# Kernel tuning notes

Hardware: AMD Instinct MI355X
Metric: run time of the kernel (lower is better)

## Reference

```python
import jax, jax.numpy as jnp
import numpy as np

C = 768      # channel
H = 6        # height = 4 + 2*pre_step
W = 6        # width  = 4 + 2*pre_step
NB = 3       # n_block = H/2
SPLIT = 6    # = width
LS = 1536    # lstm_size = C * H / NB
NH = 4       # attention heads
DM = 512     # attention d_model
DK = DM // NH
B = 256


def setup_inputs() -> dict:
    key = jax.random.key(0)
    ks = jax.random.split(key, 20)
    s_l = 1.0 / np.sqrt(LS)
    s_a = 1.0 / np.sqrt(C)
    s_o = 1.0 / np.sqrt(DM)
    u = lambda k, shape, s: jax.random.uniform(k, shape, jnp.float32, -s, s)
    return {
        "x": jax.random.normal(ks[0], (B, H * W, C), jnp.float32),
        # 2-layer LSTM encoder (input=hidden=LS), torch gate order i,f,g,o
        "enc_Wih": u(ks[1], (2, 4 * LS, LS), s_l),
        "enc_Whh": u(ks[2], (2, 4 * LS, LS), s_l),
        "enc_bih": u(ks[3], (2, 4 * LS), s_l),
        "enc_bhh": u(ks[4], (2, 4 * LS), s_l),
        # 2-layer LSTM decoder
        "dec_Wih": u(ks[5], (2, 4 * LS, LS), s_l),
        "dec_Whh": u(ks[6], (2, 4 * LS, LS), s_l),
        "dec_bih": u(ks[7], (2, 4 * LS), s_l),
        "dec_bhh": u(ks[8], (2, 4 * LS), s_l),
        # multi-head attention: 768 -> 512 (4 heads x 128) -> 768
        "Wq": u(ks[9], (C, DM), s_a), "bq": u(ks[10], (DM,), s_a),
        "Wk": u(ks[11], (C, DM), s_a), "bk": u(ks[12], (DM,), s_a),
        "Wv": u(ks[13], (C, DM), s_a), "bv": u(ks[14], (DM,), s_a),
        "Wo": u(ks[15], (DM, C), s_o), "bo": u(ks[16], (C,), s_o),
        # LayerNorm over channel
        "ln_g": jnp.ones((C,), jnp.float32),
        "ln_b": jnp.zeros((C,), jnp.float32),
    }


def _cell(x, h, c, Wi, Wh, bi, bh):
    g = x @ Wi.T + bi + h @ Wh.T + bh
    i, f, gg, o = jnp.split(g, 4, axis=-1)
    c = jax.nn.sigmoid(f) * c + jax.nn.sigmoid(i) * jnp.tanh(gg)
    h = jax.nn.sigmoid(o) * jnp.tanh(c)
    return h, c


def _step2(st, xt, Wih, Whh, bih, bhh):
    # one timestep of a 2-layer LSTM
    h0, c0, h1, c1 = st
    h0, c0 = _cell(xt, h0, c0, Wih[0], Whh[0], bih[0], bhh[0])
    h1, c1 = _cell(h0, h1, c1, Wih[1], Whh[1], bih[1], bhh[1])
    return (h0, c0, h1, c1), h1


def _forward(x, enc_Wih, enc_Whh, enc_bih, enc_bhh,
             dec_Wih, dec_Whh, dec_bih, dec_bhh,
             Wq, bq, Wk, bk, Wv, bv, Wo, bo, ln_g, ln_b):
    Bx = x.shape[0]
    xb = x.reshape(Bx, NB, 2, W, C)
    # per block, each column j is a single-timestep feature concatenating the 2 rows
    # -> time-major sequence (SPLIT, NB*Bx, LS), blocks folded into the batch dim
    seq = jnp.transpose(xb, (3, 1, 0, 2, 4)).reshape(W, NB * Bx, LS)
    z = jnp.zeros((NB * Bx, LS), x.dtype)
    carry0 = (z, z, z, z)
    # encoder consumes columns in reversed order (j = split-1 .. 0)
    enc_st, enc_ys = jax.lax.scan(
        lambda s, xt: _step2(s, xt, enc_Wih, enc_Whh, enc_bih, enc_bhh),
        carry0, seq[::-1])
    en_out = enc_ys[-1]

    def dec_step(carry, _):
        st, inp = carry
        st, out = _step2(st, inp, dec_Wih, dec_Whh, dec_bih, dec_bhh)
        return (st, out), out
    _, dec_ys = jax.lax.scan(dec_step, (enc_st, en_out), None, length=SPLIT)

    # dec_ys: (SPLIT, NB*Bx, LS) -> xout_total: (NB, Bx, 2, SPLIT, C)
    xout = dec_ys.reshape(SPLIT, NB, Bx, 2, C).transpose(1, 2, 3, 0, 4)
    xt = xout.reshape(NB, Bx, 2 * SPLIT, C)

    # neighbor-block q/k, own-block v (NB=3): i=0 -> (q1,k2,v0); i=1 -> (q0,k2,v1); i=2 -> (q1,k0,v2)
    q = xt[jnp.array([1, 0, 1])]
    k = xt[jnp.array([2, 2, 0])]
    v = xt
    T = 2 * SPLIT
    Q = (q @ Wq + bq).reshape(NB, Bx, T, NH, DK)
    K = (k @ Wk + bk).reshape(NB, Bx, T, NH, DK)
    V = (v @ Wv + bv).reshape(NB, Bx, T, NH, DK)
    scores = jnp.einsum('nbqhd,nbkhd->nbhqk', Q, K) / np.float32(np.sqrt(DK))
    att = jax.nn.softmax(scores, axis=-1)
    o = jnp.einsum('nbhqk,nbkhd->nbqhd', att, V).reshape(NB, Bx, T, DM)
    o = o @ Wo + bo  # (NB, Bx, T, C)

    # concat blocks along height, layernorm over channel
    feat = o.reshape(NB, Bx, 2, W, C).transpose(1, 0, 2, 3, 4).reshape(Bx, H * W, C)
    mu = feat.mean(-1, keepdims=True)
    var = feat.var(-1, keepdims=True)
    feature = (feat - mu) / jnp.sqrt(var + 1e-5) * ln_g + ln_b
    out_decode = feature.reshape(Bx, H, W, C)[:, 1:5, 1:5, :]
    return feature, out_decode


def reference(x, enc_Wih, enc_Whh, enc_bih, enc_bhh,
              dec_Wih, dec_Whh, dec_bih, dec_bhh,
              Wq, bq, Wk, bk, Wv, bv, Wo, bo, ln_g, ln_b):
    return _forward(x, enc_Wih, enc_Whh, enc_bih, enc_bhh,
                    dec_Wih, dec_Whh, dec_bih, dec_bhh,
                    Wq, bq, Wk, bk, Wv, bv, Wo, bo, ln_g, ln_b)
```

## Files before the change

kernel.cpp:

```cpp
#include <hip/hip_runtime.h>


typedef unsigned short u16;
typedef unsigned int   u32;
typedef __bf16 bf16x8 __attribute__((ext_vector_type(8)));
typedef short  short8 __attribute__((ext_vector_type(8)));
typedef float  f32x4  __attribute__((ext_vector_type(4)));

__device__ __forceinline__ u16 f2bf(float f) {
  u32 u = __float_as_uint(f);
  u32 r = u + 0x7FFFu + ((u >> 16) & 1u);
  return (u16)(r >> 16);
}

__device__ __forceinline__ f32x4 mfma16(short8 a, short8 b, f32x4 c) {
  return __builtin_amdgcn_mfma_f32_16x16x32_bf16(
      __builtin_bit_cast(bf16x8, a), __builtin_bit_cast(bf16x8, b), c, 0, 0, 0);
}

__device__ __forceinline__ void gload16(const u16* g, u16* l) {
  __builtin_amdgcn_global_load_lds(
      (const __attribute__((address_space(1))) u32*)g,
      (__attribute__((address_space(3))) u32*)l, 16, 0, 0);
}

__global__ __launch_bounds__(384) void lstm_cell(
    const u16* __restrict__ X, const u16* __restrict__ H,
    const u16* __restrict__ Wih, const u16* __restrict__ Whh,
    const float* __restrict__ bi, const float* __restrict__ bh,
    float* __restrict__ c, u16* __restrict__ hout, u16* __restrict__ h2)
{
  __shared__ __align__(16) u16 smem[36864];
  const int tid  = threadIdx.x;
  const int wid   = (blockIdx.x & 7) * 32 + (blockIdx.x >> 3);
  const int strip = wid >> 3;
  const int bm    = wid & 7;
  const int strip48 = strip * 48;
  const int lane = tid & 63, wave = tid >> 6;
  const int t  = wave % 3;
  const int mh = wave / 3;
  const int r16  = lane & 15, kg = lane >> 4;
  const int srow = lane >> 2, sslot = lane & 3;

  f32x4 acc[3][4];
#pragma unroll
  for (int mi = 0; mi < 3; ++mi)
#pragma unroll
    for (int g = 0; g < 4; ++g) acc[mi][g] = (f32x4)0.0f;

  auto stage = [&](int s) {
    const int slot = s & 3;
    const u16* A = (s < 48) ? X : H;
    const u16* W = (s < 48) ? Wih : Whh;
    const int k0 = ((s < 48) ? s : (s - 48)) << 5;
#pragma unroll
    for (int cc = 0; cc < 3; ++cc) {
      const int call = wave * 3 + cc;
      if (call < 6) {
        const int row  = call * 16 + srow;
        const int slog = sslot ^ ((row >> 1) & 3);
        gload16(A + (size_t)(bm * 96 + row) * 1536 + k0 + slog * 8,
                smem + slot * 3072 + call * 512);
      } else {
        const int rb   = (call - 6) * 16 + srow;
        const int slog = sslot ^ ((rb >> 1) & 3);
        const int g    = (call - 6) / 3;
        const int hh   = rb - g * 48;
        gload16(W + ((size_t)g * 1536 + strip48 + hh) * 1536 + k0 + slog * 8,
                smem + 12288 + slot * 6144 + (call - 6) * 512);
      }
    }
  };

  auto computeFrom = [&](int s) {
    const int slot = s & 3;
    const u16* baseA = smem + slot * 3072;
    const u16* baseB = smem + 12288 + slot * 6144;
    short8 af[3];
#pragma unroll
    for (int mi = 0; mi < 3; ++mi) {
      const int row = mh * 48 + mi * 16 + r16;
      af[mi] = *(const short8*)(baseA + row * 32 + ((kg ^ ((row >> 1) & 3)) << 3));
    }
    short8 bfr[4];
#pragma unroll
    for (int g = 0; g < 4; ++g) {
      const int rb = g * 48 + t * 16 + r16;
      bfr[g] = *(const short8*)(baseB + rb * 32 + ((kg ^ ((rb >> 1) & 3)) << 3));
    }
#pragma unroll
    for (int mi = 0; mi < 3; ++mi)
#pragma unroll
      for (int g = 0; g < 4; ++g)
        acc[mi][g] = mfma16(af[mi], bfr[g], acc[mi][g]);
  };

  stage(0); stage(1); stage(2); stage(3);

  for (int i = 0; i < 92; ++i) {
    asm volatile("s_waitcnt vmcnt(9)" ::: "memory");
    __builtin_amdgcn_sched_barrier(0);
    __builtin_amdgcn_s_barrier();
    computeFrom(i);
    __builtin_amdgcn_s_barrier();
    __builtin_amdgcn_sched_barrier(0);
    stage(i + 4);
  }
  asm volatile("s_waitcnt vmcnt(9)" ::: "memory");
  __builtin_amdgcn_sched_barrier(0);
  __builtin_amdgcn_s_barrier();
  computeFrom(92);
  __builtin_amdgcn_s_barrier();
  asm volatile("s_waitcnt vmcnt(6)" ::: "memory");
  __builtin_amdgcn_sched_barrier(0);
  __builtin_amdgcn_s_barrier();
  computeFrom(93);
  __builtin_amdgcn_s_barrier();
  asm volatile("s_waitcnt vmcnt(3)" ::: "memory");
  __builtin_amdgcn_sched_barrier(0);
  __builtin_amdgcn_s_barrier();
  computeFrom(94);
  __builtin_amdgcn_s_barrier();
  asm volatile("s_waitcnt vmcnt(0)" ::: "memory");
  __builtin_amdgcn_sched_barrier(0);
  __builtin_amdgcn_s_barrier();
  computeFrom(95);

  const int h = strip48 + t * 16 + r16;
  float bsum[4];
#pragma unroll
  for (int g = 0; g < 4; ++g)
    bsum[g] = bi[g * 1536 + h] + bh[g * 1536 + h];
#pragma unroll
  for (int mi = 0; mi < 3; ++mi) {
    const int row0 = bm * 96 + mh * 48 + mi * 16 + kg * 4;
#pragma unroll
    for (int j = 0; j < 4; ++j) {
      const float ig = acc[mi][0][j] + bsum[0];
      const float fg = acc[mi][1][j] + bsum[1];
      const float gz = acc[mi][2][j] + bsum[2];
      const float og = acc[mi][3][j] + bsum[3];
      const float si = 1.0f / (1.0f + expf(-ig));
      const float sf = 1.0f / (1.0f + expf(-fg));
      const float so = 1.0f / (1.0f + expf(-og));
      const size_t cij = (size_t)(row0 + j) * 1536 + h;
      const float cnew = sf * c[cij] + si * tanhf(gz);
      c[cij] = cnew;
      const u16 hv = f2bf(so * tanhf(cnew));
      hout[cij] = hv;
      if (h2) h2[cij] = hv;
    }
  }
}

template <int OUT_BF16, int HAS_BIAS>
__global__ __launch_bounds__(256, 2) void gemm_bt(
    const u16* __restrict__ A1, const u16* __restrict__ B1, int K1,
    const float* __restrict__ bias, void* __restrict__ Cout, int N)
{
  __shared__ __align__(16) u16 smem[16384];
  const int tid  = threadIdx.x;
  const int bn   = blockIdx.x * 128;
  const int bm   = blockIdx.y * 128;
  const int lane = tid & 63, wave = tid >> 6;
  const int wm   = (wave >> 1) * 64, wn = (wave & 1) * 64;
  const int r16  = lane & 15, kg = lane >> 4;
  const int srow = lane >> 2, sslot = lane & 3;

  f32x4 acc[4][4];
#pragma unroll
  for (int i = 0; i < 4; ++i)
#pragma unroll
    for (int j = 0; j < 4; ++j) acc[i][j] = (f32x4)0.0f;

  const int nt = K1 >> 5;
  auto stage = [&](int i, int buf) {
    const int k0 = i << 5;
#pragma unroll
    for (int cc2 = 0; cc2 < 2; ++cc2) {
      const int call = wave * 2 + cc2;
      const int row  = call * 16 + srow;
      const int slog = sslot ^ ((row >> 1) & 3);
      gload16(A1 + (size_t)(bm + row) * K1 + k0 + slog * 8, smem + buf * 4096 + call * 512);
      gload16(B1 + (size_t)(bn + row) * K1 + k0 + slog * 8, smem + 8192 + buf * 4096 + call * 512);
    }
  };

  stage(0, 0);
  __syncthreads();
  int cur = 0;
  for (int i = 0; i < nt; ++i) {
    if (i + 1 < nt) stage(i + 1, cur ^ 1);
    const u16* baseA = smem + cur * 4096;
    const u16* baseB = smem + 8192 + cur * 4096;
    short8 af[4], bfr[4];
#pragma unroll
    for (int mi = 0; mi < 4; ++mi) {
      const int row = wm + mi * 16 + r16;
      af[mi] = *(const short8*)(baseA + row * 32 + ((kg ^ ((row >> 1) & 3)) << 3));
    }
#pragma unroll
    for (int ni = 0; ni < 4; ++ni) {
      const int row = wn + ni * 16 + r16;
      bfr[ni] = *(const short8*)(baseB + row * 32 + ((kg ^ ((row >> 1) & 3)) << 3));
    }
#pragma unroll
    for (int mi = 0; mi < 4; ++mi)
#pragma unroll
      for (int ni = 0; ni < 4; ++ni)
        acc[mi][ni] = mfma16(af[mi], bfr[ni], acc[mi][ni]);
    __syncthreads();
    cur ^= 1;
  }

  const size_t Ns = (size_t)N;
#pragma unroll
  for (int ni = 0; ni < 4; ++ni) {
    const int col = bn + wn + ni * 16 + r16;
    const float bvv = HAS_BIAS ? bias[col] : 0.0f;
#pragma unroll
    for (int mi = 0; mi < 4; ++mi) {
      const int row0 = bm + wm + mi * 16 + kg * 4;
      f32x4 v = acc[mi][ni];
#pragma unroll
      for (int j = 0; j < 4; ++j) {
        const float val = v[j] + bvv;
        const size_t idx = (size_t)(row0 + j) * Ns + col;
        if (OUT_BF16) ((u16*)Cout)[idx] = f2bf(val);
        else          ((float*)Cout)[idx] = val;
      }
    }
  }
}

__global__ __launch_bounds__(256) void attn_kernel(const u16* __restrict__ P, u16* __restrict__ O)
{
  __shared__ __align__(16) u16 sQ[12 * 520];
  __shared__ __align__(16) u16 sK[12 * 520];
  __shared__ __align__(16) u16 sVT[512 * 24];
  __shared__ __align__(16) u16 sS[4 * 16 * 16];
  const int tid = threadIdx.x;
  const int nb = blockIdx.x >> 8;
  const int b  = blockIdx.x & 255;
  const int qb = (nb == 1) ? 0 : 1;
  const int kb = (nb == 2) ? 0 : 2;
  const size_t rq = ((size_t)qb * 256 + b) * 12;
  const size_t rk = ((size_t)kb * 256 + b) * 12;
  const size_t rv = ((size_t)nb * 256 + b) * 12;

  for (int e4 = tid; e4 < 1536; e4 += 256) {
    const int t  = e4 >> 7;
    const int cc = (e4 & 127) * 4;
    uint2 qv = *(const uint2*)(P + (rq + t) * 1536 + cc);
    *(uint2*)(sQ + t * 520 + cc) = qv;
    uint2 kv = *(const uint2*)(P + (rk + t) * 1536 + 512 + cc);
    *(uint2*)(sK + t * 520 + cc) = kv;
    uint2 vv = *(const uint2*)(P + (rv + t) * 1536 + 1024 + cc);
    sVT[(cc + 0) * 24 + t] = (u16)(vv.x & 0xffff);
    sVT[(cc + 1) * 24 + t] = (u16)(vv.x >> 16);
    sVT[(cc + 2) * 24 + t] = (u16)(vv.y & 0xffff);
    sVT[(cc + 3) * 24 + t] = (u16)(vv.y >> 16);
  }
  for (int i = tid; i < 2048; i += 256) sVT[(i >> 2) * 24 + 12 + (i & 3)] = 0;
  __syncthreads();

  const int lane = tid & 63, h = tid >> 6;
  const int r16 = lane & 15, kg = lane >> 4;
  const int hcol = h * 128;

  f32x4 sc = (f32x4)0.0f;
#pragma unroll
  for (int ks = 0; ks < 4; ++ks) {
    short8 aq  = (r16 < 12) ? *(const short8*)(sQ + r16 * 520 + hcol + ks * 32 + kg * 8) : (short8)0;
    short8 bk2 = (r16 < 12) ? *(const short8*)(sK + r16 * 520 + hcol + ks * 32 + kg * 8) : (short8)0;
    sc = mfma16(aq, bk2, sc);
  }
  const float scale = 0.08838834764831845f;
#pragma unroll
  for (int j = 0; j < 4; ++j) {
    float v = (r16 < 12) ? sc[j] * scale : -1e30f;
    float m = v;
#pragma unroll
    for (int d = 1; d < 16; d <<= 1) m = fmaxf(m, __shfl_xor(m, d));
    float e = expf(v - m);
    float s = e;
#pragma unroll
    for (int d = 1; d < 16; d <<= 1) s += __shfl_xor(s, d);
    sS[h * 256 + (kg * 4 + j) * 16 + r16] = f2bf(e / s);
  }
  __syncthreads();
  short8 av = (kg < 2) ? *(const short8*)(sS + h * 256 + r16 * 16 + kg * 8) : (short8)0;
#pragma unroll
  for (int dt = 0; dt < 8; ++dt) {
    short8 bv2 = (kg < 2) ? *(const short8*)(sVT + (hcol + dt * 16 + r16) * 24 + kg * 8) : (short8)0;
    f32x4 ov = mfma16(av, bv2, (f32x4)0.0f);
    if (kg < 3) {
#pragma unroll
      for (int j = 0; j < 4; ++j) {
        const int q = kg * 4 + j;
        O[(rv + q) * 512 + hcol + dt * 16 + r16] = f2bf(ov[j]);
      }
    }
  }
}

__global__ __launch_bounds__(256) void layernorm_kernel(
    const float* __restrict__ feat, const float* __restrict__ gam,
    const float* __restrict__ bet, float* __restrict__ out)
{
  const int row = blockIdx.x;
  const int b = row / 36, hidx = row - b * 36;
  const int nb = hidx / 12, t = hidx - nb * 12;
  const float* src = feat + ((size_t)nb * 3072 + b * 12 + t) * 768;
  const int tid = threadIdx.x;
  float v0 = src[tid], v1 = src[tid + 256], v2 = src[tid + 512];
  float s = v0 + v1 + v2, sq = v0 * v0 + v1 * v1 + v2 * v2;
#pragma unroll
  for (int d = 1; d < 64; d <<= 1) { s += __shfl_xor(s, d); sq += __shfl_xor(sq, d); }
  __shared__ float ps[4], pq[4];
  if ((tid & 63) == 0) { ps[tid >> 6] = s; pq[tid >> 6] = sq; }
  __syncthreads();
  s  = ps[0] + ps[1] + ps[2] + ps[3];
  sq = pq[0] + pq[1] + pq[2] + pq[3];
  const float mean = s * (1.0f / 768.0f);
  const float var  = sq * (1.0f / 768.0f) - mean * mean;
  const float rstd = rsqrtf(var + 1e-5f);
  float* dst = out + (size_t)row * 768;
  const int hh = hidx / 6, wp = hidx - hh * 6;
  float* dst2 = nullptr;
  if (hh >= 1 && hh < 5 && wp >= 1 && wp < 5)
    dst2 = out + 7077888 + ((size_t)b * 16 + (hh - 1) * 4 + (wp - 1)) * 768;
#pragma unroll
  for (int i = 0; i < 3; ++i) {
    const int cix = tid + i * 256;
    const float vv = (i == 0) ? v0 : (i == 1 ? v1 : v2);
    const float o = (vv - mean) * rstd * gam[cix] + bet[cix];
    dst[cix] = o;
    if (dst2) dst2[cix] = o;
  }
}

__global__ __launch_bounds__(256) void cast_bf16_kernel(const float* __restrict__ src,
                                                        u16* __restrict__ dst, int n4)
{
  const int i = blockIdx.x * 256 + threadIdx.x;
  if (i >= n4) return;
  float4 v = ((const float4*)src)[i];
  uint2 pk;
  pk.x = (u32)f2bf(v.x) | ((u32)f2bf(v.y) << 16);
  pk.y = (u32)f2bf(v.z) | ((u32)f2bf(v.w) << 16);
  ((uint2*)dst)[i] = pk;
}

__global__ __launch_bounds__(256) void pack_qkvT(const float* __restrict__ Wq,
    const float* __restrict__ Wk, const float* __restrict__ Wv, u16* __restrict__ dst)
{
  const int idx = blockIdx.x * 256 + threadIdx.x;
  if (idx >= 1536 * 768) return;
  const int d = idx / 768, c = idx - d * 768;
  float v;
  if (d < 512)       v = Wq[(size_t)c * 512 + d];
  else if (d < 1024) v = Wk[(size_t)c * 512 + d - 512];
  else               v = Wv[(size_t)c * 512 + d - 1024];
  dst[idx] = f2bf(v);
}

__global__ __launch_bounds__(256) void pack_bias(const float* __restrict__ bq,
    const float* __restrict__ bk, const float* __restrict__ bv, float* __restrict__ dst)
{
  const int i = blockIdx.x * 256 + threadIdx.x;
  if (i < 512)       dst[i] = bq[i];
  else if (i < 1024) dst[i] = bk[i - 512];
  else if (i < 1536) dst[i] = bv[i - 1024];
}

__global__ __launch_bounds__(256) void pack_WoT(const float* __restrict__ Wo, u16* __restrict__ dst)
{
  const int idx = blockIdx.x * 256 + threadIdx.x;
  if (idx >= 768 * 512) return;
  const int n = idx / 512, k = idx - n * 512;
  dst[idx] = f2bf(Wo[(size_t)k * 768 + n]);
}

__global__ __launch_bounds__(256) void build_Xe(const float* __restrict__ x, u16* __restrict__ Xe)
{
  const int i4 = blockIdx.x * 256 + threadIdx.x;
  if (i4 >= 1769472) return;
  const int e = i4 * 4;
  const int c = e % 768;
  const int r2 = (e / 768) & 1;
  const int r = (e / 1536) % 768;
  const int s = e / 1179648;
  const int nb = r >> 8, bb = r & 255;
  const int w = 5 - s;
  const float* src = x + ((size_t)bb * 36 + (nb * 2 + r2) * 6 + w) * 768 + c;
  float4 v = *(const float4*)src;
  uint2 pk;
  pk.x = (u32)f2bf(v.x) | ((u32)f2bf(v.y) << 16);
  pk.y = (u32)f2bf(v.z) | ((u32)f2bf(v.w) << 16);
  ((uint2*)Xe)[i4] = pk;
}

__global__ __launch_bounds__(256) void build_xt(const u16* __restrict__ decys, u16* __restrict__ xt)
{
  const int i4 = blockIdx.x * 256 + threadIdx.x;
  if (i4 >= 1769472) return;
  const int e = i4 * 4;
  const int c = e % 768;
  const int t = (e / 768) % 12;
  const int b = (e / 9216) % 256;
  const int nb = e / 2359296;
  const int r2 = t / 6, s = t - r2 * 6;
  const u16* src = decys + ((size_t)s * 768 + nb * 256 + b) * 1536 + r2 * 768 + c;
  ((uint2*)xt)[i4] = *(const uint2*)src;
}

extern "C" void kernel_launch(void* const* d_in, const int* in_sizes, int n_in,
                              void* d_out, int out_size, void* d_ws, size_t ws_size,
                              hipStream_t stream)
{
  const float* x    = (const float*)d_in[0];
  const float* eWih = (const float*)d_in[1];
  const float* eWhh = (const float*)d_in[2];
  const float* ebih = (const float*)d_in[3];
  const float* ebhh = (const float*)d_in[4];
  const float* dWih = (const float*)d_in[5];
  const float* dWhh = (const float*)d_in[6];
  const float* dbih = (const float*)d_in[7];
  const float* dbhh = (const float*)d_in[8];
  const float* Wq = (const float*)d_in[9];
  const float* bq = (const float*)d_in[10];
  const float* Wk = (const float*)d_in[11];
  const float* bk = (const float*)d_in[12];
  const float* Wv = (const float*)d_in[13];
  const float* bv = (const float*)d_in[14];
  const float* Wo = (const float*)d_in[15];
  const float* bo = (const float*)d_in[16];
  const float* lng = (const float*)d_in[17];
  const float* lnb = (const float*)d_in[18];

  char* ws = (char*)d_ws;
  const size_t WBYTES = 37748736;
  u16* Weih = (u16*)(ws);
  u16* Wehh = (u16*)(ws + WBYTES);
  u16* Wdih = (u16*)(ws + 2 * WBYTES);
  u16* Wdhh = (u16*)(ws + 3 * WBYTES);
  u16*   xtb   = (u16*)(ws);
  u16*   Pqkv  = (u16*)(ws + 14155776);
  u16*   Obuf  = (u16*)(ws + 14155776 + 28311552);
  float* feato = (float*)(ws + 14155776 + 28311552 + 9437184);
  size_t off = 4 * WBYTES;
  auto take = [&](size_t bytes) -> char* {
    char* p = ws + off;
    off = (off + bytes + 255) & ~(size_t)255;
    return p;
  };
  u16* Wqkv  = (u16*)take((size_t)1536 * 768 * 2);
  float* bqkv = (float*)take(1536 * 4);
  u16* WoT   = (u16*)take((size_t)768 * 512 * 2);
  u16* Xe    = (u16*)take((size_t)6 * 768 * 1536 * 2);
  u16* h0a   = (u16*)take((size_t)768 * 1536 * 2);
  u16* h0b   = (u16*)take((size_t)768 * 1536 * 2);
  u16* h1a   = (u16*)take((size_t)768 * 1536 * 2);
  u16* h1b   = (u16*)take((size_t)768 * 1536 * 2);
  float* c0  = (float*)take((size_t)768 * 1536 * 4);
  float* c1  = (float*)take((size_t)768 * 1536 * 4);
  u16* decys = (u16*)take((size_t)6 * 768 * 1536 * 2);
  if (off > ws_size) return;

  const size_t WL = (size_t)6144 * 1536;
  const dim3 blk(256);
  const dim3 blkCell(384);

  cast_bf16_kernel<<<18432, blk, 0, stream>>>(eWih, Weih, 4718592);
  cast_bf16_kernel<<<18432, blk, 0, stream>>>(eWhh, Wehh, 4718592);
  cast_bf16_kernel<<<18432, blk, 0, stream>>>(dWih, Wdih, 4718592);
  cast_bf16_kernel<<<18432, blk, 0, stream>>>(dWhh, Wdhh, 4718592);
  pack_qkvT<<<4608, blk, 0, stream>>>(Wq, Wk, Wv, Wqkv);
  pack_bias<<<6, blk, 0, stream>>>(bq, bk, bv, bqkv);
  pack_WoT<<<1536, blk, 0, stream>>>(Wo, WoT);
  build_Xe<<<6912, blk, 0, stream>>>(x, Xe);

  hipMemsetAsync(h0a, 0, (size_t)768 * 1536 * 2, stream);
  hipMemsetAsync(h1a, 0, (size_t)768 * 1536 * 2, stream);
  hipMemsetAsync(c0, 0, (size_t)768 * 1536 * 4, stream);
  hipMemsetAsync(c1, 0, (size_t)768 * 1536 * 4, stream);

  u16* h0[2] = {h0a, h0b};
  u16* h1[2] = {h1a, h1b};
  int p = 0;
  for (int s = 0; s < 6; ++s) {
    lstm_cell<<<256, blkCell, 0, stream>>>(Xe + (size_t)s * 768 * 1536, h0[p],
                                           Weih, Wehh, ebih, ebhh, c0, h0[p ^ 1], nullptr);
    lstm_cell<<<256, blkCell, 0, stream>>>(h0[p ^ 1], h1[p],
                                           Weih + WL, Wehh + WL, ebih + 6144, ebhh + 6144,
                                           c1, h1[p ^ 1], nullptr);
    p ^= 1;
  }
  for (int t = 0; t < 6; ++t) {
    lstm_cell<<<256, blkCell, 0, stream>>>(h1[p], h0[p],
                                           Wdih, Wdhh, dbih, dbhh, c0, h0[p ^ 1], nullptr);
    lstm_cell<<<256, blkCell, 0, stream>>>(h0[p ^ 1], h1[p],
                                           Wdih + WL, Wdhh + WL, dbih + 6144, dbhh + 6144,
                                           c1, h1[p ^ 1], decys + (size_t)t * 768 * 1536);
    p ^= 1;
  }
  build_xt<<<6912, blk, 0, stream>>>(decys, xtb);
  gemm_bt<1, 1><<<dim3(12, 72), blk, 0, stream>>>(xtb, Wqkv, 768, bqkv, Pqkv, 1536);
  attn_kernel<<<768, blk, 0, stream>>>(Pqkv, Obuf);
  gemm_bt<0, 1><<<dim3(6, 72), blk, 0, stream>>>(Obuf, WoT, 512, bo, feato, 768);
  layernorm_kernel<<<9216, blk, 0, stream>>>(feato, lng, lnb, (float*)d_out);
}
```

Before: 1.448 ms.

## Double K-tile depth to 64 with 3-stage LDS pipeline in LSTM cell GEMM

Widens each K stage from 32 to 64 elements and switches the LDS ring from 4 slots to 3, halving the number of barrier-synchronized iterations and giving each wave twice as many MFMAs per barrier pair. The LDS swizzle changes to an 8-slot XOR pattern to suit 128-byte rows. The cost is more LDS per block (about 108KB), which may limit occupancy, a shallower prefetch depth in stages, and more registers for fragments.

```diff
diff --git a/kernel.cpp b/kernel.cpp
--- a/kernel.cpp
+++ b/kernel.cpp
@@ -30,7 +30,7 @@
     const float* __restrict__ bi, const float* __restrict__ bh,
     float* __restrict__ c, u16* __restrict__ hout, u16* __restrict__ h2)
 {
-  __shared__ __align__(16) u16 smem[36864];
+  __shared__ __align__(16) u16 smem[55296];
   const int tid  = threadIdx.x;
   const int wid   = (blockIdx.x & 7) * 32 + (blockIdx.x >> 3);
   const int strip = wid >> 3;
@@ -40,7 +40,7 @@
   const int t  = wave % 3;
   const int mh = wave / 3;
   const int r16  = lane & 15, kg = lane >> 4;
-  const int srow = lane >> 2, sslot = lane & 3;
+  const int srow8 = lane >> 3, sl = lane & 7;
 
   f32x4 acc[3][4];
 #pragma unroll
@@ -48,83 +48,87 @@
 #pragma unroll
     for (int g = 0; g < 4; ++g) acc[mi][g] = (f32x4)0.0f;
 
+  const int slog = sl ^ srow8;
   auto stage = [&](int s) {
-    const int slot = s & 3;
-    const u16* A = (s < 48) ? X : H;
-    const u16* W = (s < 48) ? Wih : Whh;
-    const int k0 = ((s < 48) ? s : (s - 48)) << 5;
-#pragma unroll
-    for (int cc = 0; cc < 3; ++cc) {
-      const int call = wave * 3 + cc;
-      if (call < 6) {
-        const int row  = call * 16 + srow;
-        const int slog = sslot ^ ((row >> 1) & 3);
-        gload16(A + (size_t)(bm * 96 + row) * 1536 + k0 + slog * 8,
-                smem + slot * 3072 + call * 512);
+    const int slot = s % 3;
+    const u16* Aptr = (s < 24) ? X : H;
+    const u16* W    = (s < 24) ? Wih : Whh;
+    const int k0 = ((s < 24) ? s : (s - 24)) << 6;
+#pragma unroll
+    for (int cc = 0; cc < 6; ++cc) {
+      const int call = wave * 6 + cc;
+      if (call < 12) {
+        const int row = call * 8 + srow8;
+        gload16(Aptr + (size_t)(bm * 96 + row) * 1536 + k0 + slog * 8,
+                smem + slot * 6144 + call * 512);
       } else {
-        const int rb   = (call - 6) * 16 + srow;
-        const int slog = sslot ^ ((rb >> 1) & 3);
-        const int g    = (call - 6) / 3;
-        const int hh   = rb - g * 48;
+        const int cb  = call - 12;
+        const int rb  = cb * 8 + srow8;
+        const int g   = cb / 6;
+        const int hh  = rb - g * 48;
         gload16(W + ((size_t)g * 1536 + strip48 + hh) * 1536 + k0 + slog * 8,
-                smem + 12288 + slot * 6144 + (call - 6) * 512);
+                smem + 18432 + slot * 12288 + cb * 512);
       }
     }
   };
 
   auto computeFrom = [&](int s) {
-    const int slot = s & 3;
-    const u16* baseA = smem + slot * 3072;
-    const u16* baseB = smem + 12288 + slot * 6144;
-    short8 af[3];
+    const int slot = s % 3;
+    const u16* baseA = smem + slot * 6144;
+    const u16* baseB = smem + 18432 + slot * 12288;
+    short8 af[3][2], bfr[4][2];
 #pragma unroll
     for (int mi = 0; mi < 3; ++mi) {
       const int row = mh * 48 + mi * 16 + r16;
-      af[mi] = *(const short8*)(baseA + row * 32 + ((kg ^ ((row >> 1) & 3)) << 3));
-    }
-    short8 bfr[4];
+#pragma unroll
+      for (int kf = 0; kf < 2; ++kf) {
+        const int sx = (kf * 4 + kg) ^ (row & 7);
+        af[mi][kf] = *(const short8*)(baseA + row * 64 + sx * 8);
+      }
+    }
 #pragma unroll
     for (int g = 0; g < 4; ++g) {
       const int rb = g * 48 + t * 16 + r16;
-      bfr[g] = *(const short8*)(baseB + rb * 32 + ((kg ^ ((rb >> 1) & 3)) << 3));
-    }
-#pragma unroll
-    for (int mi = 0; mi < 3; ++mi)
-#pragma unroll
-      for (int g = 0; g < 4; ++g)
-        acc[mi][g] = mfma16(af[mi], bfr[g], acc[mi][g]);
+#pragma unroll
+      for (int kf = 0; kf < 2; ++kf) {
+        const int sx = (kf * 4 + kg) ^ (rb & 7);
+        bfr[g][kf] = *(const short8*)(baseB + rb * 64 + sx * 8);
+      }
+    }
+#pragma unroll
+    for (int kf = 0; kf < 2; ++kf)
+#pragma unroll
+      for (int mi = 0; mi < 3; ++mi)
+#pragma unroll
+        for (int g = 0; g < 4; ++g)
+          acc[mi][g] = mfma16(af[mi][kf], bfr[g][kf], acc[mi][g]);
   };
 
-  stage(0); stage(1); stage(2); stage(3);
-
-  for (int i = 0; i < 92; ++i) {
-    asm volatile("s_waitcnt vmcnt(9)" ::: "memory");
+  stage(0); stage(1); stage(2);
+
+  for (int i = 0; i < 45; ++i) {
+    asm volatile("s_waitcnt vmcnt(12)" ::: "memory");
     __builtin_amdgcn_sched_barrier(0);
     __builtin_amdgcn_s_barrier();
     computeFrom(i);
     __builtin_amdgcn_s_barrier();
     __builtin_amdgcn_sched_barrier(0);
-    stage(i + 4);
-  }
-  asm volatile("s_waitcnt vmcnt(9)" ::: "memory");
+    stage(i + 3);
+  }
+  asm volatile("s_waitcnt vmcnt(12)" ::: "memory");
   __builtin_amdgcn_sched_barrier(0);
   __builtin_amdgcn_s_barrier();
-  computeFrom(92);
+  computeFrom(45);
   __builtin_amdgcn_s_barrier();
   asm volatile("s_waitcnt vmcnt(6)" ::: "memory");
   __builtin_amdgcn_sched_barrier(0);
   __builtin_amdgcn_s_barrier();
-  computeFrom(93);
-  __builtin_amdgcn_s_barrier();
-  asm volatile("s_waitcnt vmcnt(3)" ::: "memory");
-  __builtin_amdgcn_sched_barrier(0);
-  __builtin_amdgcn_s_barrier();
-  computeFrom(94);
+  computeFrom(46);
   __builtin_amdgcn_s_barrier();
   asm volatile("s_waitcnt vmcnt(0)" ::: "memory");
   __builtin_amdgcn_sched_barrier(0);
   __builtin_amdgcn_s_barrier();
-  computeFrom(95);
+  computeFrom(47);
 
   const int h = strip48 + t * 16 + r16;
   float bsum[4];
```

Measured after the change: 1.366 ms. -5.7%, faster.

## Retile LSTM cell GEMM to 128-row blocks with 4 waves and 192 workgroups

Applied to the files above, without the earlier changes.

Changes the fused LSTM-cell GEMM tile from 96 rows x 192 gate columns with 6 waves to 128 rows x 192 gate columns with 4 waves. Each wave now owns 32 rows across all 12 gate fragments, and the grid shrinks from 256 to 192 workgroups. This raises MFMA work per LDS fragment load and cuts redundant weight streaming per block. In exchange it uses more accumulator registers and leaves fewer workgroups than the 256 CUs, so some CUs sit idle. It also drops the trailing barriers in the pipeline epilogue.

```diff
diff --git a/kernel.cpp b/kernel.cpp
--- a/kernel.cpp
+++ b/kernel.cpp
@@ -24,81 +24,80 @@
       (__attribute__((address_space(3))) u32*)l, 16, 0, 0);
 }
 
-__global__ __launch_bounds__(384) void lstm_cell(
+__global__ __launch_bounds__(256) void lstm_cell(
     const u16* __restrict__ X, const u16* __restrict__ H,
     const u16* __restrict__ Wih, const u16* __restrict__ Whh,
     const float* __restrict__ bi, const float* __restrict__ bh,
     float* __restrict__ c, u16* __restrict__ hout, u16* __restrict__ h2)
 {
-  __shared__ __align__(16) u16 smem[36864];
+  __shared__ __align__(16) u16 smem[40960];
   const int tid  = threadIdx.x;
-  const int wid   = (blockIdx.x & 7) * 32 + (blockIdx.x >> 3);
-  const int strip = wid >> 3;
-  const int bm    = wid & 7;
+  const int wid   = (blockIdx.x & 7) * 24 + (blockIdx.x >> 3);
+  const int strip = wid / 6;
+  const int bm    = wid - strip * 6;
   const int strip48 = strip * 48;
   const int lane = tid & 63, wave = tid >> 6;
-  const int t  = wave % 3;
-  const int mh = wave / 3;
   const int r16  = lane & 15, kg = lane >> 4;
   const int srow = lane >> 2, sslot = lane & 3;
 
-  f32x4 acc[3][4];
-#pragma unroll
-  for (int mi = 0; mi < 3; ++mi)
-#pragma unroll
-    for (int g = 0; g < 4; ++g) acc[mi][g] = (f32x4)0.0f;
+  f32x4 acc[2][12];
+#pragma unroll
+  for (int mi = 0; mi < 2; ++mi)
+#pragma unroll
+    for (int nf = 0; nf < 12; ++nf) acc[mi][nf] = (f32x4)0.0f;
 
   auto stage = [&](int s) {
     const int slot = s & 3;
-    const u16* A = (s < 48) ? X : H;
-    const u16* W = (s < 48) ? Wih : Whh;
+    const u16* Aptr = (s < 48) ? X : H;
+    const u16* W    = (s < 48) ? Wih : Whh;
     const int k0 = ((s < 48) ? s : (s - 48)) << 5;
 #pragma unroll
-    for (int cc = 0; cc < 3; ++cc) {
-      const int call = wave * 3 + cc;
-      if (call < 6) {
+    for (int cc = 0; cc < 5; ++cc) {
+      const int call = wave * 5 + cc;
+      if (call < 8) {
         const int row  = call * 16 + srow;
         const int slog = sslot ^ ((row >> 1) & 3);
-        gload16(A + (size_t)(bm * 96 + row) * 1536 + k0 + slog * 8,
-                smem + slot * 3072 + call * 512);
+        gload16(Aptr + (size_t)(bm * 128 + row) * 1536 + k0 + slog * 8,
+                smem + slot * 4096 + call * 512);
       } else {
-        const int rb   = (call - 6) * 16 + srow;
+        const int cb   = call - 8;
+        const int rb   = cb * 16 + srow;
+        const int g    = cb / 3;
+        const int hh   = (cb - g * 3) * 16 + srow;
         const int slog = sslot ^ ((rb >> 1) & 3);
-        const int g    = (call - 6) / 3;
-        const int hh   = rb - g * 48;
         gload16(W + ((size_t)g * 1536 + strip48 + hh) * 1536 + k0 + slog * 8,
-                smem + 12288 + slot * 6144 + (call - 6) * 512);
+                smem + 16384 + slot * 6144 + cb * 512);
       }
     }
   };
 
   auto computeFrom = [&](int s) {
     const int slot = s & 3;
-    const u16* baseA = smem + slot * 3072;
-    const u16* baseB = smem + 12288 + slot * 6144;
-    short8 af[3];
-#pragma unroll
-    for (int mi = 0; mi < 3; ++mi) {
-      const int row = mh * 48 + mi * 16 + r16;
+    const u16* baseA = smem + slot * 4096;
+    const u16* baseB = smem + 16384 + slot * 6144;
+    short8 af[2];
+#pragma unroll
+    for (int mi = 0; mi < 2; ++mi) {
+      const int row = wave * 32 + mi * 16 + r16;
       af[mi] = *(const short8*)(baseA + row * 32 + ((kg ^ ((row >> 1) & 3)) << 3));
     }
-    short8 bfr[4];
-#pragma unroll
-    for (int g = 0; g < 4; ++g) {
-      const int rb = g * 48 + t * 16 + r16;
-      bfr[g] = *(const short8*)(baseB + rb * 32 + ((kg ^ ((rb >> 1) & 3)) << 3));
-    }
-#pragma unroll
-    for (int mi = 0; mi < 3; ++mi)
-#pragma unroll
-      for (int g = 0; g < 4; ++g)
-        acc[mi][g] = mfma16(af[mi], bfr[g], acc[mi][g]);
+    short8 bfr[12];
+#pragma unroll
+    for (int nf = 0; nf < 12; ++nf) {
+      const int rb = nf * 16 + r16;
+      bfr[nf] = *(const short8*)(baseB + rb * 32 + ((kg ^ ((rb >> 1) & 3)) << 3));
+    }
+#pragma unroll
+    for (int mi = 0; mi < 2; ++mi)
+#pragma unroll
+      for (int nf = 0; nf < 12; ++nf)
+        acc[mi][nf] = mfma16(af[mi], bfr[nf], acc[mi][nf]);
   };
 
   stage(0); stage(1); stage(2); stage(3);
 
   for (int i = 0; i < 92; ++i) {
-    asm volatile("s_waitcnt vmcnt(9)" ::: "memory");
+    asm volatile("s_waitcnt vmcnt(15)" ::: "memory");
     __builtin_amdgcn_sched_barrier(0);
     __builtin_amdgcn_s_barrier();
     computeFrom(i);
@@ -106,49 +105,49 @@
     __builtin_amdgcn_sched_barrier(0);
     stage(i + 4);
   }
-  asm volatile("s_waitcnt vmcnt(9)" ::: "memory");
+  asm volatile("s_waitcnt vmcnt(15)" ::: "memory");
   __builtin_amdgcn_sched_barrier(0);
   __builtin_amdgcn_s_barrier();
   computeFrom(92);
-  __builtin_amdgcn_s_barrier();
-  asm volatile("s_waitcnt vmcnt(6)" ::: "memory");
+  asm volatile("s_waitcnt vmcnt(10)" ::: "memory");
   __builtin_amdgcn_sched_barrier(0);
   __builtin_amdgcn_s_barrier();
   computeFrom(93);
-  __builtin_amdgcn_s_barrier();
-  asm volatile("s_waitcnt vmcnt(3)" ::: "memory");
+  asm volatile("s_waitcnt vmcnt(5)" ::: "memory");
   __builtin_amdgcn_sched_barrier(0);
   __builtin_amdgcn_s_barrier();
   computeFrom(94);
-  __builtin_amdgcn_s_barrier();
   asm volatile("s_waitcnt vmcnt(0)" ::: "memory");
   __builtin_amdgcn_sched_barrier(0);
   __builtin_amdgcn_s_barrier();
   computeFrom(95);
 
-  const int h = strip48 + t * 16 + r16;
-  float bsum[4];
-#pragma unroll
-  for (int g = 0; g < 4; ++g)
-    bsum[g] = bi[g * 1536 + h] + bh[g * 1536 + h];
-#pragma unroll
-  for (int mi = 0; mi < 3; ++mi) {
-    const int row0 = bm * 96 + mh * 48 + mi * 16 + kg * 4;
-#pragma unroll
-    for (int j = 0; j < 4; ++j) {
-      const float ig = acc[mi][0][j] + bsum[0];
-      const float fg = acc[mi][1][j] + bsum[1];
-      const float gz = acc[mi][2][j] + bsum[2];
-      const float og = acc[mi][3][j] + bsum[3];
-      const float si = 1.0f / (1.0f + expf(-ig));
-      const float sf = 1.0f / (1.0f + expf(-fg));
-      const float so = 1.0f / (1.0f + expf(-og));
-      const size_t cij = (size_t)(row0 + j) * 1536 + h;
-      const float cnew = sf * c[cij] + si * tanhf(gz);
-      c[cij] = cnew;
-      const u16 hv = f2bf(so * tanhf(cnew));
-      hout[cij] = hv;
-      if (h2) h2[cij] = hv;
+#pragma unroll
+  for (int t3 = 0; t3 < 3; ++t3) {
+    const int h = strip48 + t3 * 16 + r16;
+    float bsum[4];
+#pragma unroll
+    for (int g = 0; g < 4; ++g)
+      bsum[g] = bi[g * 1536 + h] + bh[g * 1536 + h];
+#pragma unroll
+    for (int mi = 0; mi < 2; ++mi) {
+      const int row0 = bm * 128 + wave * 32 + mi * 16 + kg * 4;
+#pragma unroll
+      for (int j = 0; j < 4; ++j) {
+        const float ig = acc[mi][0 + t3][j] + bsum[0];
+        const float fg = acc[mi][3 + t3][j] + bsum[1];
+        const float gz = acc[mi][6 + t3][j] + bsum[2];
+        const float og = acc[mi][9 + t3][j] + bsum[3];
+        const float si = 1.0f / (1.0f + expf(-ig));
+        const float sf = 1.0f / (1.0f + expf(-fg));
+        const float so = 1.0f / (1.0f + expf(-og));
+        const size_t cij = (size_t)(row0 + j) * 1536 + h;
+        const float cnew = sf * c[cij] + si * tanhf(gz);
+        c[cij] = cnew;
+        const u16 hv = f2bf(so * tanhf(cnew));
+        hout[cij] = hv;
+        if (h2) h2[cij] = hv;
+      }
     }
   }
 }
@@ -470,7 +469,6 @@
 
   const size_t WL = (size_t)6144 * 1536;
   const dim3 blk(256);
-  const dim3 blkCell(384);
 
   cast_bf16_kernel<<<18432, blk, 0, stream>>>(eWih, Weih, 4718592);
   cast_bf16_kernel<<<18432, blk, 0, stream>>>(eWhh, Wehh, 4718592);
@@ -490,19 +488,19 @@
   u16* h1[2] = {h1a, h1b};
   int p = 0;
   for (int s = 0; s < 6; ++s) {
-    lstm_cell<<<256, blkCell, 0, stream>>>(Xe + (size_t)s * 768 * 1536, h0[p],
-                                           Weih, Wehh, ebih, ebhh, c0, h0[p ^ 1], nullptr);
-    lstm_cell<<<256, blkCell, 0, stream>>>(h0[p ^ 1], h1[p],
-                                           Weih + WL, Wehh + WL, ebih + 6144, ebhh + 6144,
-                                           c1, h1[p ^ 1], nullptr);
+    lstm_cell<<<192, blk, 0, stream>>>(Xe + (size_t)s * 768 * 1536, h0[p],
+                                       Weih, Wehh, ebih, ebhh, c0, h0[p ^ 1], nullptr);
+    lstm_cell<<<192, blk, 0, stream>>>(h0[p ^ 1], h1[p],
+                                       Weih + WL, Wehh + WL, ebih + 6144, ebhh + 6144,
+                                       c1, h1[p ^ 1], nullptr);
     p ^= 1;
   }
   for (int t = 0; t < 6; ++t) {
-    lstm_cell<<<256, blkCell, 0, stream>>>(h1[p], h0[p],
-                                           Wdih, Wdhh, dbih, dbhh, c0, h0[p ^ 1], nullptr);
-    lstm_cell<<<256, blkCell, 0, stream>>>(h0[p ^ 1], h1[p],
-                                           Wdih + WL, Wdhh + WL, dbih + 6144, dbhh + 6144,
-                                           c1, h1[p ^ 1], decys + (size_t)t * 768 * 1536);
+    lstm_cell<<<192, blk, 0, stream>>>(h1[p], h0[p],
+                                       Wdih, Wdhh, dbih, dbhh, c0, h0[p ^ 1], nullptr);
+    lstm_cell<<<192, blk, 0, stream>>>(h0[p ^ 1], h1[p],
+                                       Wdih + WL, Wdhh + WL, dbih + 6144, dbhh + 6144,
+                                       c1, h1[p ^ 1], decys + (size_t)t * 768 * 1536);
     p ^= 1;
   }
   build_xt<<<6912, blk, 0, stream>>>(decys, xtb);
```

Result: slower. 1.964 ms (+35.6%).

## Split LSTM cell tile across eight waves and stage gates through LDS

Applied to the files above, without the earlier changes.

The LSTM cell kernel grows from 6 to 8 waves per block. Each wave now computes a 3x3 grid of MFMA tiles inside one gate, instead of a 3x4 grid spanning all four gates. Global-to-LDS loads are split so two waves load the activation tile and six waves load weight rows, with a per-wave vmcnt wait to match. Because each wave no longer holds all four gates for its outputs, gate pre-activations are written to LDS and the elementwise cell update is redone with a flat, coalesced thread mapping. The aim is better latency hiding and coalesced c/h traffic, at the cost of more LDS fragment reads, an extra LDS round trip and an extra block barrier.

```diff
diff --git a/kernel.cpp b/kernel.cpp
--- a/kernel.cpp
+++ b/kernel.cpp
@@ -24,7 +24,7 @@
       (__attribute__((address_space(3))) u32*)l, 16, 0, 0);
 }
 
-__global__ __launch_bounds__(384) void lstm_cell(
+__global__ __launch_bounds__(512) void lstm_cell(
     const u16* __restrict__ X, const u16* __restrict__ H,
     const u16* __restrict__ Wih, const u16* __restrict__ Whh,
     const float* __restrict__ bi, const float* __restrict__ bh,
@@ -32,42 +32,45 @@
 {
   __shared__ __align__(16) u16 smem[36864];
   const int tid  = threadIdx.x;
-  const int wid   = (blockIdx.x & 7) * 32 + (blockIdx.x >> 3);
+  const int wid   = ((blockIdx.x & 7) << 5) + (blockIdx.x >> 3);
   const int strip = wid >> 3;
   const int bm    = wid & 7;
   const int strip48 = strip * 48;
   const int lane = tid & 63, wave = tid >> 6;
-  const int t  = wave % 3;
-  const int mh = wave / 3;
+  const int gq = wave >> 1, mh = wave & 1;
   const int r16  = lane & 15, kg = lane >> 4;
   const int srow = lane >> 2, sslot = lane & 3;
 
-  f32x4 acc[3][4];
+  f32x4 acc[3][3];
 #pragma unroll
   for (int mi = 0; mi < 3; ++mi)
 #pragma unroll
-    for (int g = 0; g < 4; ++g) acc[mi][g] = (f32x4)0.0f;
+    for (int ni = 0; ni < 3; ++ni) acc[mi][ni] = (f32x4)0.0f;
 
   auto stage = [&](int s) {
     const int slot = s & 3;
-    const u16* A = (s < 48) ? X : H;
-    const u16* W = (s < 48) ? Wih : Whh;
+    const u16* Aptr = (s < 48) ? X : H;
+    const u16* W    = (s < 48) ? Wih : Whh;
     const int k0 = ((s < 48) ? s : (s - 48)) << 5;
-#pragma unroll
-    for (int cc = 0; cc < 3; ++cc) {
-      const int call = wave * 3 + cc;
-      if (call < 6) {
+    if (wave < 2) {
+#pragma unroll
+      for (int cc = 0; cc < 3; ++cc) {
+        const int call = wave * 3 + cc;
         const int row  = call * 16 + srow;
         const int slog = sslot ^ ((row >> 1) & 3);
-        gload16(A + (size_t)(bm * 96 + row) * 1536 + k0 + slog * 8,
+        gload16(Aptr + (size_t)(bm * 96 + row) * 1536 + k0 + slog * 8,
                 smem + slot * 3072 + call * 512);
-      } else {
-        const int rb   = (call - 6) * 16 + srow;
+      }
+    } else {
+#pragma unroll
+      for (int cc = 0; cc < 2; ++cc) {
+        const int cb   = (wave - 2) * 2 + cc;
+        const int rb   = cb * 16 + srow;
+        const int g    = cb / 3;
+        const int hh   = rb - g * 48;
         const int slog = sslot ^ ((rb >> 1) & 3);
-        const int g    = (call - 6) / 3;
-        const int hh   = rb - g * 48;
         gload16(W + ((size_t)g * 1536 + strip48 + hh) * 1536 + k0 + slog * 8,
-                smem + 12288 + slot * 6144 + (call - 6) * 512);
+                smem + 12288 + slot * 6144 + cb * 512);
       }
     }
   };
@@ -82,23 +85,24 @@
       const int row = mh * 48 + mi * 16 + r16;
       af[mi] = *(const short8*)(baseA + row * 32 + ((kg ^ ((row >> 1) & 3)) << 3));
     }
-    short8 bfr[4];
-#pragma unroll
-    for (int g = 0; g < 4; ++g) {
-      const int rb = g * 48 + t * 16 + r16;
-      bfr[g] = *(const short8*)(baseB + rb * 32 + ((kg ^ ((rb >> 1) & 3)) << 3));
+    short8 bfr[3];
+#pragma unroll
+    for (int ni = 0; ni < 3; ++ni) {
+      const int rb = gq * 48 + ni * 16 + r16;
+      bfr[ni] = *(const short8*)(baseB + rb * 32 + ((kg ^ ((rb >> 1) & 3)) << 3));
     }
 #pragma unroll
     for (int mi = 0; mi < 3; ++mi)
 #pragma unroll
-      for (int g = 0; g < 4; ++g)
-        acc[mi][g] = mfma16(af[mi], bfr[g], acc[mi][g]);
+      for (int ni = 0; ni < 3; ++ni)
+        acc[mi][ni] = mfma16(af[mi], bfr[ni], acc[mi][ni]);
   };
 
   stage(0); stage(1); stage(2); stage(3);
 
   for (int i = 0; i < 92; ++i) {
-    asm volatile("s_waitcnt vmcnt(9)" ::: "memory");
+    if (wave < 2) asm volatile("s_waitcnt vmcnt(9)" ::: "memory");
+    else          asm volatile("s_waitcnt vmcnt(6)" ::: "memory");
     __builtin_amdgcn_sched_barrier(0);
     __builtin_amdgcn_s_barrier();
     computeFrom(i);
@@ -106,50 +110,59 @@
     __builtin_amdgcn_sched_barrier(0);
     stage(i + 4);
   }
-  asm volatile("s_waitcnt vmcnt(9)" ::: "memory");
+  if (wave < 2) asm volatile("s_waitcnt vmcnt(9)" ::: "memory");
+  else          asm volatile("s_waitcnt vmcnt(6)" ::: "memory");
   __builtin_amdgcn_sched_barrier(0);
   __builtin_amdgcn_s_barrier();
   computeFrom(92);
-  __builtin_amdgcn_s_barrier();
-  asm volatile("s_waitcnt vmcnt(6)" ::: "memory");
+  if (wave < 2) asm volatile("s_waitcnt vmcnt(6)" ::: "memory");
+  else          asm volatile("s_waitcnt vmcnt(4)" ::: "memory");
   __builtin_amdgcn_sched_barrier(0);
   __builtin_amdgcn_s_barrier();
   computeFrom(93);
-  __builtin_amdgcn_s_barrier();
-  asm volatile("s_waitcnt vmcnt(3)" ::: "memory");
+  if (wave < 2) asm volatile("s_waitcnt vmcnt(3)" ::: "memory");
+  else          asm volatile("s_waitcnt vmcnt(2)" ::: "memory");
   __builtin_amdgcn_sched_barrier(0);
   __builtin_amdgcn_s_barrier();
   computeFrom(94);
-  __builtin_amdgcn_s_barrier();
   asm volatile("s_waitcnt vmcnt(0)" ::: "memory");
   __builtin_amdgcn_sched_barrier(0);
   __builtin_amdgcn_s_barrier();
   computeFrom(95);
-
-  const int h = strip48 + t * 16 + r16;
-  float bsum[4];
-#pragma unroll
-  for (int g = 0; g < 4; ++g)
-    bsum[g] = bi[g * 1536 + h] + bh[g * 1536 + h];
-#pragma unroll
-  for (int mi = 0; mi < 3; ++mi) {
-    const int row0 = bm * 96 + mh * 48 + mi * 16 + kg * 4;
-#pragma unroll
-    for (int j = 0; j < 4; ++j) {
-      const float ig = acc[mi][0][j] + bsum[0];
-      const float fg = acc[mi][1][j] + bsum[1];
-      const float gz = acc[mi][2][j] + bsum[2];
-      const float og = acc[mi][3][j] + bsum[3];
-      const float si = 1.0f / (1.0f + expf(-ig));
-      const float sf = 1.0f / (1.0f + expf(-fg));
-      const float so = 1.0f / (1.0f + expf(-og));
-      const size_t cij = (size_t)(row0 + j) * 1536 + h;
-      const float cnew = sf * c[cij] + si * tanhf(gz);
-      c[cij] = cnew;
-      const u16 hv = f2bf(so * tanhf(cnew));
-      hout[cij] = hv;
-      if (h2) h2[cij] = hv;
-    }
+  __builtin_amdgcn_s_barrier();
+
+  float* sG = (float*)smem;
+#pragma unroll
+  for (int mi = 0; mi < 3; ++mi)
+#pragma unroll
+    for (int ni = 0; ni < 3; ++ni)
+#pragma unroll
+      for (int j = 0; j < 4; ++j) {
+        const int row = mh * 48 + mi * 16 + kg * 4 + j;
+        const int h   = ni * 16 + r16;
+        sG[gq * 4608 + row * 48 + h] = acc[mi][ni][j];
+      }
+  __syncthreads();
+
+#pragma unroll
+  for (int k = 0; k < 9; ++k) {
+    const int e   = tid + k * 512;
+    const int row = e / 48;
+    const int h   = e - row * 48;
+    const int hg  = strip48 + h;
+    const float ig = sG[e]            + bi[hg]        + bh[hg];
+    const float fg = sG[4608 + e]     + bi[1536 + hg] + bh[1536 + hg];
+    const float gz = sG[9216 + e]     + bi[3072 + hg] + bh[3072 + hg];
+    const float og = sG[13824 + e]    + bi[4608 + hg] + bh[4608 + hg];
+    const float si = 1.0f / (1.0f + expf(-ig));
+    const float sf = 1.0f / (1.0f + expf(-fg));
+    const float so = 1.0f / (1.0f + expf(-og));
+    const size_t cij = (size_t)(bm * 96 + row) * 1536 + hg;
+    const float cnew = sf * c[cij] + si * tanhf(gz);
+    c[cij] = cnew;
+    const u16 hv = f2bf(so * tanhf(cnew));
+    hout[cij] = hv;
+    if (h2) h2[cij] = hv;
   }
 }
 
@@ -470,7 +483,7 @@
 
   const size_t WL = (size_t)6144 * 1536;
   const dim3 blk(256);
-  const dim3 blkCell(384);
+  const dim3 blkCell(512);
 
   cast_bf16_kernel<<<18432, blk, 0, stream>>>(eWih, Weih, 4718592);
   cast_bf16_kernel<<<18432, blk, 0, stream>>>(eWhh, Wehh, 4718592);
```

After: 1.350 ms. -6.8%, faster.
